# Kernel optimization log

Measured on AMD Instinct MI355X. Metric: run time of the kernel, lower is better.

The kernel has to match this reference:

```python
import jax, jax.numpy as jnp
import numpy as np

BC = 256      # block_channel
RC = 64       # reduced_channel = BC // 4
NB0, NB1 = 4, 3   # num_blocks per modality (1024/256, 768/256)
TB = NB0 + NB1    # total_blocks
EPS = 1e-5        # BatchNorm eps (eval mode, running_mean=0, running_var=1)
LOWEST = 0.0      # lowest_atten


def setup_inputs() -> dict:
    key = jax.random.key(0)
    k = jax.random.split(key, 4)
    B, T = 8, 4096
    x0 = jax.random.normal(k[0], (B, 1024, T), jnp.float32)
    x1 = jax.random.normal(k[1], (B, 768, T), jnp.float32)
    W1 = jax.random.normal(k[2], (BC, RC), jnp.float32) / np.sqrt(BC).astype(np.float32)
    b1 = jnp.zeros((RC,), jnp.float32)
    gamma = jnp.ones((RC,), jnp.float32)
    beta = jnp.zeros((RC,), jnp.float32)
    Wh = jax.random.normal(k[3], (TB, RC, BC), jnp.float32) / np.sqrt(RC).astype(np.float32)
    bh = jnp.zeros((TB, BC), jnp.float32)
    return {"x0": x0, "x1": x1, "W1": W1, "b1": b1, "gamma": gamma,
            "beta": beta, "Wh": Wh, "bh": bh}


def reference(x0, x1, W1, b1, gamma, beta, Wh, bh):
    B, _, T = x0.shape
    # split channels into blocks: [B, nb, BC, T]
    xr0 = x0.reshape(B, NB0, BC, T)
    xr1 = x1.reshape(B, NB1, BC, T)
    # block-sum over blocks, then global average pool over time -> [B, BC]
    gap = xr0.sum(axis=1).mean(axis=-1) + xr1.sum(axis=1).mean(axis=-1)
    # joint projector: Linear -> BatchNorm1d(eval: mean=0, var=1) -> ReLU
    h = gap @ W1 + b1
    h = jnp.maximum(h * (gamma / jnp.sqrt(1.0 + EPS)) + beta, 0.0)  # [B, RC]
    # all TB attention heads as one grouped GEMM: [TB, B, BC]
    scores = jnp.einsum('br,krc->kbc', h, Wh) + bh[:, None, :]
    att = jax.nn.softmax(scores, axis=0)          # softmax over block axis (dim=0)
    att = jnp.transpose(att, (1, 0, 2))           # [B, TB, BC]
    att = LOWEST + att * (1.0 - LOWEST)
    # scale each block's features
    out0 = (xr0 * att[:, :NB0, :, None]).reshape(x0.shape)
    out1 = (xr1 * att[:, NB0:, :, None]).reshape(x1.shape)
    return (out0, out1)
```

## Files before the change

kernel.cpp:

```cpp
#include <hip/hip_runtime.h>
#include <hip/hip_bf16.h>

#define B_SZ 8
#define T_SZ 4096
#define BC 256
#define RC 64
#define NB0 4
#define NB1 3
#define TB 7
#define ROWS0 (B_SZ * 1024)
#define ROWS1 (B_SZ * 768)
#define ROWS_TOTAL (ROWS0 + ROWS1)
#define X0_ELEMS (33554432ull)

__global__ __launch_bounds__(256) void gap_kernel(const float* __restrict__ x0,
                                                  const float* __restrict__ x1,
                                                  float* __restrict__ gap) {
    const int gtid = blockIdx.x * blockDim.x + threadIdx.x;
    const int wave = gtid >> 6;
    const int lane = threadIdx.x & 63;

    const float4* src;
    int b, c;
    if (wave < ROWS0) {
        b = wave >> 10;
        const int ch = wave & 1023;
        c = ch & 255;
        src = (const float4*)(x0 + (size_t)wave * T_SZ);
    } else {
        const int r = wave - ROWS0;
        b = r / 768;
        const int ch = r - b * 768;
        c = ch & 255;
        src = (const float4*)(x1 + (size_t)r * T_SZ);
    }

    float sum = 0.0f;
#pragma unroll
    for (int it = 0; it < 16; ++it) {
        float4 v = src[it * 64 + lane];
        sum += (v.x + v.y) + (v.z + v.w);
    }
#pragma unroll
    for (int off = 32; off > 0; off >>= 1)
        sum += __shfl_down(sum, off, 64);

    if (lane == 0)
        atomicAdd(gap + b * BC + c, sum * (1.0f / (float)T_SZ));
}

__global__ __launch_bounds__(256) void attn_kernel(const float* __restrict__ gap,
                                                   const float* __restrict__ W1,
                                                   const float* __restrict__ b1,
                                                   const float* __restrict__ gamma,
                                                   const float* __restrict__ beta,
                                                   const float* __restrict__ Wh,
                                                   const float* __restrict__ bh,
                                                   float* __restrict__ att) {
    __shared__ float s_gap[B_SZ][BC];
    __shared__ float s_h[B_SZ][RC];
    const int tid = threadIdx.x;

#pragma unroll
    for (int b = 0; b < B_SZ; ++b)
        s_gap[b][tid] = gap[b * BC + tid];
    __syncthreads();

    const float bnscale = rsqrtf(1.0f + 1e-5f);
    for (int p = tid; p < B_SZ * RC; p += 256) {
        const int b = p >> 6;
        const int r = p & 63;
        float acc = 0.0f;
        for (int c = 0; c < BC; ++c)
            acc = fmaf(s_gap[b][c], W1[c * RC + r], acc);
        acc += b1[r];
        acc = acc * (gamma[r] * bnscale) + beta[r];
        s_h[b][r] = fmaxf(acc, 0.0f);
    }
    __syncthreads();

    float sc[TB];
#pragma unroll 1
    for (int b = 0; b < B_SZ; ++b) {
        float mx = -1e30f;
#pragma unroll
        for (int k = 0; k < TB; ++k) {
            float acc = bh[k * BC + tid];
            for (int r = 0; r < RC; ++r)
                acc = fmaf(s_h[b][r], Wh[(k * RC + r) * BC + tid], acc);
            sc[k] = acc;
            mx = fmaxf(mx, acc);
        }
        float sum = 0.0f;
#pragma unroll
        for (int k = 0; k < TB; ++k) {
            sc[k] = __expf(sc[k] - mx);
            sum += sc[k];
        }
        const float inv = 1.0f / sum;
#pragma unroll
        for (int k = 0; k < TB; ++k)
            att[(b * TB + k) * BC + tid] = sc[k] * inv;
    }
}

__global__ __launch_bounds__(256) void scale_kernel(const float* __restrict__ x0,
                                                    const float* __restrict__ x1,
                                                    const float* __restrict__ att,
                                                    float* __restrict__ out) {
    const int row = blockIdx.x;
    const float4* src;
    float4* dst;
    float a;
    if (row < ROWS0) {
        const int b = row >> 10;
        const int ch = row & 1023;
        a = att[(b * TB + (ch >> 8)) * BC + (ch & 255)];
        src = (const float4*)(x0 + (size_t)row * T_SZ);
        dst = (float4*)(out + (size_t)row * T_SZ);
    } else {
        const int r = row - ROWS0;
        const int b = r / 768;
        const int ch = r - b * 768;
        a = att[(b * TB + NB0 + (ch >> 8)) * BC + (ch & 255)];
        src = (const float4*)(x1 + (size_t)r * T_SZ);
        dst = (float4*)(out + X0_ELEMS + (size_t)r * T_SZ);
    }
    const int tid = threadIdx.x;
#pragma unroll
    for (int it = 0; it < 4; ++it) {
        float4 v = src[it * 256 + tid];
        v.x *= a; v.y *= a; v.z *= a; v.w *= a;
        dst[it * 256 + tid] = v;
    }
}

extern "C" void kernel_launch(void* const* d_in, const int* in_sizes, int n_in,
                              void* d_out, int out_size, void* d_ws, size_t ws_size,
                              hipStream_t stream) {
    const float* x0    = (const float*)d_in[0];
    const float* x1    = (const float*)d_in[1];
    const float* W1    = (const float*)d_in[2];
    const float* b1    = (const float*)d_in[3];
    const float* gamma = (const float*)d_in[4];
    const float* beta  = (const float*)d_in[5];
    const float* Wh    = (const float*)d_in[6];
    const float* bh    = (const float*)d_in[7];
    float* out = (float*)d_out;

    float* gap = (float*)d_ws;
    float* att = gap + 2048;

    hipMemsetAsync(gap, 0, B_SZ * BC * sizeof(float), stream);

    gap_kernel<<<ROWS_TOTAL / 4, 256, 0, stream>>>(x0, x1, gap);
    attn_kernel<<<1, 256, 0, stream>>>(gap, W1, b1, gamma, beta, Wh, bh, att);
    scale_kernel<<<ROWS_TOTAL, 256, 0, stream>>>(x0, x1, att, out);
}
```

Before: 467.9 us.

## Split attention into per-head score blocks, fuse softmax into scale kernel

The row-sum kernel now writes plain per-row sums into the start of the output buffer, which removes the memset and the atomics. The single-block attention kernel becomes a 7-block score kernel, one block per head, that rebuilds the GAP from the row sums and computes raw scores for all batches. The softmax over heads moves into the scale kernel, where each row recomputes its own attention weight. Output stores use non-temporal hints. The serial single-block work shrinks, but every row now repeats a small softmax, and reusing the output as scratch relies on the later scale kernel overwriting it.

```diff
diff --git a/kernel.cpp b/kernel.cpp
--- a/kernel.cpp
+++ b/kernel.cpp
@@ -1,5 +1,4 @@
 #include <hip/hip_runtime.h>
-#include <hip/hip_bf16.h>
 
 #define B_SZ 8
 #define T_SZ 4096
@@ -13,27 +12,18 @@
 #define ROWS_TOTAL (ROWS0 + ROWS1)
 #define X0_ELEMS (33554432ull)
 
-__global__ __launch_bounds__(256) void gap_kernel(const float* __restrict__ x0,
-                                                  const float* __restrict__ x1,
-                                                  float* __restrict__ gap) {
-    const int gtid = blockIdx.x * blockDim.x + threadIdx.x;
+typedef float vfloat4 __attribute__((ext_vector_type(4)));
+
+__global__ __launch_bounds__(256) void rowsum_kernel(const float* __restrict__ x0,
+                                                     const float* __restrict__ x1,
+                                                     float* __restrict__ rowsum) {
+    const int gtid = blockIdx.x * 256 + threadIdx.x;
     const int wave = gtid >> 6;
     const int lane = threadIdx.x & 63;
 
-    const float4* src;
-    int b, c;
-    if (wave < ROWS0) {
-        b = wave >> 10;
-        const int ch = wave & 1023;
-        c = ch & 255;
-        src = (const float4*)(x0 + (size_t)wave * T_SZ);
-    } else {
-        const int r = wave - ROWS0;
-        b = r / 768;
-        const int ch = r - b * 768;
-        c = ch & 255;
-        src = (const float4*)(x1 + (size_t)r * T_SZ);
-    }
+    const float4* src = (wave < ROWS0)
+        ? (const float4*)(x0 + (size_t)wave * T_SZ)
+        : (const float4*)(x1 + (size_t)(wave - ROWS0) * T_SZ);
 
     float sum = 0.0f;
 #pragma unroll
@@ -46,92 +36,114 @@
         sum += __shfl_down(sum, off, 64);
 
     if (lane == 0)
-        atomicAdd(gap + b * BC + c, sum * (1.0f / (float)T_SZ));
+        rowsum[wave] = sum;
 }
 
-__global__ __launch_bounds__(256) void attn_kernel(const float* __restrict__ gap,
-                                                   const float* __restrict__ W1,
-                                                   const float* __restrict__ b1,
-                                                   const float* __restrict__ gamma,
-                                                   const float* __restrict__ beta,
-                                                   const float* __restrict__ Wh,
-                                                   const float* __restrict__ bh,
-                                                   float* __restrict__ att) {
-    __shared__ float s_gap[B_SZ][BC];
-    __shared__ float s_h[B_SZ][RC];
+__global__ __launch_bounds__(256) void score_kernel(const float* __restrict__ rowsum,
+                                                    const float* __restrict__ W1,
+                                                    const float* __restrict__ b1,
+                                                    const float* __restrict__ gamma,
+                                                    const float* __restrict__ beta,
+                                                    const float* __restrict__ Wh,
+                                                    const float* __restrict__ bh,
+                                                    float* __restrict__ scores) {
+    __shared__ float s_gap[B_SZ * BC];
+    __shared__ float s_h[B_SZ * RC];
     const int tid = threadIdx.x;
+    const int k = blockIdx.x;
 
 #pragma unroll
-    for (int b = 0; b < B_SZ; ++b)
-        s_gap[b][tid] = gap[b * BC + tid];
+    for (int p = tid; p < B_SZ * BC; p += 256) {
+        const int b = p >> 8;
+        const int c = p & 255;
+        float s = 0.0f;
+#pragma unroll
+        for (int blk = 0; blk < NB0; ++blk)
+            s += rowsum[b * 1024 + blk * 256 + c];
+#pragma unroll
+        for (int blk = 0; blk < NB1; ++blk)
+            s += rowsum[ROWS0 + b * 768 + blk * 256 + c];
+        s_gap[p] = s * (1.0f / (float)T_SZ);
+    }
     __syncthreads();
 
     const float bnscale = rsqrtf(1.0f + 1e-5f);
+#pragma unroll
     for (int p = tid; p < B_SZ * RC; p += 256) {
         const int b = p >> 6;
         const int r = p & 63;
         float acc = 0.0f;
+#pragma unroll 8
         for (int c = 0; c < BC; ++c)
-            acc = fmaf(s_gap[b][c], W1[c * RC + r], acc);
+            acc = fmaf(s_gap[b * BC + c], W1[c * RC + r], acc);
         acc += b1[r];
         acc = acc * (gamma[r] * bnscale) + beta[r];
-        s_h[b][r] = fmaxf(acc, 0.0f);
+        s_h[p] = fmaxf(acc, 0.0f);
     }
     __syncthreads();
 
-    float sc[TB];
-#pragma unroll 1
-    for (int b = 0; b < B_SZ; ++b) {
-        float mx = -1e30f;
+    float acc[B_SZ];
+    const float bias = bh[k * BC + tid];
 #pragma unroll
-        for (int k = 0; k < TB; ++k) {
-            float acc = bh[k * BC + tid];
-            for (int r = 0; r < RC; ++r)
-                acc = fmaf(s_h[b][r], Wh[(k * RC + r) * BC + tid], acc);
-            sc[k] = acc;
-            mx = fmaxf(mx, acc);
-        }
-        float sum = 0.0f;
+    for (int b = 0; b < B_SZ; ++b) acc[b] = bias;
+    for (int r = 0; r < RC; ++r) {
+        const float w = Wh[(k * RC + r) * BC + tid];
 #pragma unroll
-        for (int k = 0; k < TB; ++k) {
-            sc[k] = __expf(sc[k] - mx);
-            sum += sc[k];
-        }
-        const float inv = 1.0f / sum;
+        for (int b = 0; b < B_SZ; ++b)
+            acc[b] = fmaf(s_h[b * RC + r], w, acc[b]);
+    }
 #pragma unroll
-        for (int k = 0; k < TB; ++k)
-            att[(b * TB + k) * BC + tid] = sc[k] * inv;
-    }
+    for (int b = 0; b < B_SZ; ++b)
+        scores[(k * B_SZ + b) * BC + tid] = acc[b];
 }
 
 __global__ __launch_bounds__(256) void scale_kernel(const float* __restrict__ x0,
                                                     const float* __restrict__ x1,
-                                                    const float* __restrict__ att,
+                                                    const float* __restrict__ scores,
                                                     float* __restrict__ out) {
     const int row = blockIdx.x;
-    const float4* src;
-    float4* dst;
-    float a;
+    const vfloat4* src;
+    vfloat4* dst;
+    int b, c, ksel;
     if (row < ROWS0) {
-        const int b = row >> 10;
+        b = row >> 10;
         const int ch = row & 1023;
-        a = att[(b * TB + (ch >> 8)) * BC + (ch & 255)];
-        src = (const float4*)(x0 + (size_t)row * T_SZ);
-        dst = (float4*)(out + (size_t)row * T_SZ);
+        ksel = ch >> 8;
+        c = ch & 255;
+        src = (const vfloat4*)(x0 + (size_t)row * T_SZ);
+        dst = (vfloat4*)(out + (size_t)row * T_SZ);
     } else {
         const int r = row - ROWS0;
-        const int b = r / 768;
+        b = (int)((unsigned)r / 768u);
         const int ch = r - b * 768;
-        a = att[(b * TB + NB0 + (ch >> 8)) * BC + (ch & 255)];
-        src = (const float4*)(x1 + (size_t)r * T_SZ);
-        dst = (float4*)(out + X0_ELEMS + (size_t)r * T_SZ);
+        ksel = NB0 + (ch >> 8);
+        c = ch & 255;
+        src = (const vfloat4*)(x1 + (size_t)r * T_SZ);
+        dst = (vfloat4*)(out + X0_ELEMS + (size_t)r * T_SZ);
     }
+
+    float sc[TB];
+    float mx = -1e30f;
+#pragma unroll
+    for (int kk = 0; kk < TB; ++kk) {
+        sc[kk] = scores[(kk * B_SZ + b) * BC + c];
+        mx = fmaxf(mx, sc[kk]);
+    }
+    float sum = 0.0f, esel = 0.0f;
+#pragma unroll
+    for (int kk = 0; kk < TB; ++kk) {
+        const float e = __expf(sc[kk] - mx);
+        sum += e;
+        esel = (kk == ksel) ? e : esel;
+    }
+    const float a = esel / sum;
+
     const int tid = threadIdx.x;
 #pragma unroll
     for (int it = 0; it < 4; ++it) {
-        float4 v = src[it * 256 + tid];
-        v.x *= a; v.y *= a; v.z *= a; v.w *= a;
-        dst[it * 256 + tid] = v;
+        vfloat4 v = src[it * 256 + tid];
+        v *= a;
+        __builtin_nontemporal_store(v, &dst[it * 256 + tid]);
     }
 }
 
@@ -148,12 +160,10 @@
     const float* bh    = (const float*)d_in[7];
     float* out = (float*)d_out;
 
-    float* gap = (float*)d_ws;
-    float* att = gap + 2048;
+    float* rowsum = out;
+    float* scores = (float*)d_ws;
 
-    hipMemsetAsync(gap, 0, B_SZ * BC * sizeof(float), stream);
-
-    gap_kernel<<<ROWS_TOTAL / 4, 256, 0, stream>>>(x0, x1, gap);
-    attn_kernel<<<1, 256, 0, stream>>>(gap, W1, b1, gamma, beta, Wh, bh, att);
-    scale_kernel<<<ROWS_TOTAL, 256, 0, stream>>>(x0, x1, att, out);
+    rowsum_kernel<<<ROWS_TOTAL / 4, 256, 0, stream>>>(x0, x1, rowsum);
+    score_kernel<<<TB, 256, 0, stream>>>(rowsum, W1, b1, gamma, beta, Wh, bh, scores);
+    scale_kernel<<<ROWS_TOTAL, 256, 0, stream>>>(x0, x1, scores, out);
 }
```

Result: faster. 455.6 us (-2.6%).
